# Performance work log

Measured on AMD Instinct MI355X. Metric: run time of the kernel, lower is better.

## Reference

```python
import jax, jax.numpy as jnp
import numpy as np


def _conv1x1(x_flat, W, b):
    # x_flat: [B, Cin, N], W: [Cout, Cin], b: [Cout]
    return jnp.einsum('oc,bcn->bon', W, x_flat) + b[None, :, None]


def setup_inputs() -> dict:
    key = jax.random.key(0)
    ks = jax.random.split(key, 7)
    B, C, H, W = 8, 64, 64, 64
    Ch = C // 2
    s_in = 1.0 / np.sqrt(C)
    x = jax.random.normal(ks[0], (B, C, H, W), dtype=jnp.float32)
    Wb = jax.random.uniform(ks[1], (Ch, C), jnp.float32, -s_in, s_in)
    bb = jax.random.uniform(ks[2], (Ch,), jnp.float32, -s_in, s_in)
    Wc = jax.random.uniform(ks[3], (Ch, C), jnp.float32, -s_in, s_in)
    bc = jax.random.uniform(ks[4], (Ch,), jnp.float32, -s_in, s_in)
    Wd = jax.random.uniform(ks[5], (C, C), jnp.float32, -s_in, s_in)
    bd = jax.random.uniform(ks[6], (C,), jnp.float32, -s_in, s_in)
    return {'x': x, 'Wb': Wb, 'bb': bb, 'Wc': Wc, 'bc': bc, 'Wd': Wd, 'bd': bd}


def reference(x, Wb, bb, Wc, bc, Wd, bd):
    B, C, H, Wd_ = x.shape
    N = H * Wd_
    x_flat = x.reshape(B, C, N)
    feat_b = _conv1x1(x_flat, Wb, bb)            # [B, C/2, N]
    feat_c = _conv1x1(x_flat, Wc, bc)            # [B, C/2, N]
    # scores[b,n,m] = sum_c feat_b[b,c,n] * feat_c[b,c,m]
    scores = jnp.einsum('bcn,bcm->bnm', feat_b, feat_c)
    attn = jax.nn.softmax(scores, axis=-1)       # [B, N, N]
    feat_d = _conv1x1(x_flat, Wd, bd)            # [B, C, N]
    # feat_e[b,c,m] = sum_n feat_d[b,c,n] * attn[b,m,n]  (bmm with attn^T)
    feat_e = jnp.einsum('bcn,bmn->bcm', feat_d, attn)
    return feat_e.reshape(B, C, H, Wd_) + x
```

## Files before the change

### kernel.cpp

```cpp
#include <hip/hip_runtime.h>

#define N_TOK 4096
#define L2E 1.44269504088896340736f

typedef short bf16x8 __attribute__((ext_vector_type(8)));
typedef float f32x4 __attribute__((ext_vector_type(4)));
typedef float f32x16 __attribute__((ext_vector_type(16)));
typedef unsigned int u32x4 __attribute__((ext_vector_type(4)));
typedef unsigned short u16x4 __attribute__((ext_vector_type(4)));

static __device__ __forceinline__ unsigned short f2bf(float f) {
    unsigned int u = __builtin_bit_cast(unsigned int, f);
    u += 0x7FFFu + ((u >> 16) & 1u);
    return (unsigned short)(u >> 16);
}
static __device__ __forceinline__ float bf2f(unsigned short v) {
    return __builtin_bit_cast(float, ((unsigned)v) << 16);
}

__global__ __launch_bounds__(256) void proj_kernel(
    const float* __restrict__ x,
    const float* __restrict__ Wb, const float* __restrict__ bb,
    const float* __restrict__ Wc, const float* __restrict__ bc,
    const float* __restrict__ Wd, const float* __restrict__ bd,
    unsigned short* __restrict__ Qg, unsigned short* __restrict__ Kg,
    unsigned short* __restrict__ VgT)
{
    const int b   = blockIdx.y;
    const int n0  = blockIdx.x * 64;
    const int tid = threadIdx.x;

    __shared__ unsigned short Wl[128 * 72];
    __shared__ unsigned short xT[64 * 72];
    __shared__ float bl[128];

    #pragma unroll
    for (int i = 0; i < 32; ++i) {
        int e = i * 256 + tid;
        int row = e >> 6, c = e & 63;
        float v;
        if (row < 32)      v = Wb[row * 64 + c];
        else if (row < 64) v = Wc[(row - 32) * 64 + c];
        else               v = Wd[(row - 64) * 64 + c];
        Wl[row * 72 + c] = f2bf(v);
    }
    if (tid < 128) {
        float v;
        if (tid < 32)      v = bb[tid];
        else if (tid < 64) v = bc[tid - 32];
        else               v = bd[tid - 64];
        bl[tid] = v;
    }
    #pragma unroll
    for (int i = 0; i < 16; ++i) {
        int e = i * 256 + tid;
        int c = e >> 6, nn = e & 63;
        xT[nn * 72 + c] = f2bf(x[((b * 64 + c) << 12) + n0 + nn]);
    }
    __syncthreads();

    const int w = tid >> 6, l = tid & 63;
    const int lrow = l & 15, lk = (l >> 4) * 8;

    const f32x4 vzero = {0.f, 0.f, 0.f, 0.f};
    f32x4 acc[2][4];
    #pragma unroll
    for (int rt = 0; rt < 2; ++rt)
        #pragma unroll
        for (int ct = 0; ct < 4; ++ct)
            acc[rt][ct] = vzero;

    #pragma unroll
    for (int kb = 0; kb < 2; ++kb) {
        bf16x8 af[2];
        #pragma unroll
        for (int rt = 0; rt < 2; ++rt)
            af[rt] = *(const bf16x8*)&Wl[(w * 32 + rt * 16 + lrow) * 72 + kb * 32 + lk];
        #pragma unroll
        for (int ct = 0; ct < 4; ++ct) {
            bf16x8 bfr = *(const bf16x8*)&xT[(ct * 16 + lrow) * 72 + kb * 32 + lk];
            #pragma unroll
            for (int rt = 0; rt < 2; ++rt)
                acc[rt][ct] = __builtin_amdgcn_mfma_f32_16x16x32_bf16(af[rt], bfr, acc[rt][ct], 0, 0, 0);
        }
    }

    #pragma unroll
    for (int rt = 0; rt < 2; ++rt) {
        const int row0 = w * 32 + rt * 16 + ((l >> 4) << 2);
        #pragma unroll
        for (int ct = 0; ct < 4; ++ct) {
            const int n = n0 + ct * 16 + lrow;
            if (row0 < 64) {
                u16x4 pk;
                #pragma unroll
                for (int r = 0; r < 4; ++r) {
                    float v = acc[rt][ct][r] + bl[row0 + r];
                    if (row0 < 32) v *= L2E;
                    pk[r] = f2bf(v);
                }
                unsigned short* dst = (row0 < 32)
                    ? Qg + (size_t)(b * N_TOK + n) * 32 + row0
                    : Kg + (size_t)(b * N_TOK + n) * 32 + (row0 - 32);
                *(u16x4*)dst = pk;
            } else {
                #pragma unroll
                for (int r = 0; r < 4; ++r)
                    VgT[((size_t)(b * 64 + row0 - 64 + r) << 12) + n] =
                        f2bf(acc[rt][ct][r] + bl[row0 + r]);
            }
        }
    }
}

template <int NHALF>
__global__ __launch_bounds__(256) void attn_kernel(
    const unsigned short* __restrict__ Qg,
    const unsigned short* __restrict__ Kg,
    const unsigned short* __restrict__ VgT,
    const float* __restrict__ x,
    float* __restrict__ outp,
    unsigned short* __restrict__ Opart,
    float* __restrict__ Ppart)
{
    const int nwg = 256 * NHALF;
    int i = blockIdx.x;
    int wg = (i & 7) * (nwg >> 3) + (i >> 3);
    const int b    = wg / (32 * NHALF);
    const int rem  = wg % (32 * NHALF);
    const int half = (NHALF >= 2) ? (rem >> 5) : 0;
    const int qblk = (NHALF >= 2) ? (rem & 31) : rem;
    const int q0   = qblk * 128;
    const int jbase = half * (N_TOK / NHALF);
    const int NT    = (N_TOK / NHALF) / 64;

    const int tid = threadIdx.x;
    const int w  = tid >> 6, l = tid & 63;
    const int lc = l & 31, hi = l >> 5;

    __shared__ __align__(16) unsigned short Kl[2][64 * 36];
    __shared__ __align__(16) unsigned short Vt[2][64 * 68];
    __shared__ float den[4][32];

    const unsigned short* qp = Qg + (size_t)(b * N_TOK + q0 + w * 32 + lc) * 32 + hi * 8;
    const bf16x8 qf0 = *(const bf16x8*)qp;
    const bf16x8 qf1 = *(const bf16x8*)(qp + 16);

    const int kj = tid >> 2, kseg = (tid & 3) * 8;
    const int vc = tid >> 2, vj   = (tid & 3) * 16;
    const size_t kbase = (size_t)(b * N_TOK + jbase + kj) * 32 + kseg;
    const size_t vbase = ((size_t)(b * 64 + vc) << 12) + jbase + vj;

    u32x4 kreg, vreg0, vreg1;

    kreg  = *(const u32x4*)&Kg[kbase];
    vreg0 = *(const u32x4*)&VgT[vbase];
    vreg1 = *(const u32x4*)&VgT[vbase + 8];
    *(u32x4*)&Kl[0][kj * 36 + kseg]   = kreg;
    *(u32x4*)&Vt[0][vc * 68 + vj]     = vreg0;
    *(u32x4*)&Vt[0][vc * 68 + vj + 8] = vreg1;
    if (NT > 1) {
        kreg  = *(const u32x4*)&Kg[kbase + 64 * 32];
        vreg0 = *(const u32x4*)&VgT[vbase + 64];
        vreg1 = *(const u32x4*)&VgT[vbase + 64 + 8];
    }
    __syncthreads();

    const f32x16 z16 = {0.f,0.f,0.f,0.f,0.f,0.f,0.f,0.f,0.f,0.f,0.f,0.f,0.f,0.f,0.f,0.f};
    f32x16 o0 = z16, o1 = z16;
    f32x16 s0, s1;
    float ps0 = 0.f, ps1 = 0.f;

    {
        __builtin_amdgcn_s_setprio(1);
        bf16x8 a00 = *(const bf16x8*)&Kl[0][(lc) * 36 + hi * 8];
        bf16x8 a01 = *(const bf16x8*)&Kl[0][(lc) * 36 + 16 + hi * 8];
        bf16x8 a10 = *(const bf16x8*)&Kl[0][(32 + lc) * 36 + hi * 8];
        bf16x8 a11 = *(const bf16x8*)&Kl[0][(32 + lc) * 36 + 16 + hi * 8];
        s0 = __builtin_amdgcn_mfma_f32_32x32x16_bf16(a00, qf0, z16, 0, 0, 0);
        s0 = __builtin_amdgcn_mfma_f32_32x32x16_bf16(a01, qf1, s0, 0, 0, 0);
        s1 = __builtin_amdgcn_mfma_f32_32x32x16_bf16(a10, qf0, z16, 0, 0, 0);
        s1 = __builtin_amdgcn_mfma_f32_32x32x16_bf16(a11, qf1, s1, 0, 0, 0);
        __builtin_amdgcn_s_setprio(0);
    }

    for (int t = 0; t < NT; ++t) {
        const int cur = t & 1;

        if (t + 1 < NT) {
            *(u32x4*)&Kl[cur ^ 1][kj * 36 + kseg]   = kreg;
            *(u32x4*)&Vt[cur ^ 1][vc * 68 + vj]     = vreg0;
            *(u32x4*)&Vt[cur ^ 1][vc * 68 + vj + 8] = vreg1;
        }
        if (t + 2 < NT) {
            const int j2 = (t + 2) * 64;
            kreg  = *(const u32x4*)&Kg[kbase + (size_t)j2 * 32];
            vreg0 = *(const u32x4*)&VgT[vbase + j2];
            vreg1 = *(const u32x4*)&VgT[vbase + j2 + 8];
        }

        #pragma unroll
        for (int kb = 0; kb < 4; ++kb) {
            const f32x16& sv = (kb >> 1) ? s1 : s0;
            const int e = (kb & 1) * 8;
            float p[8];
            #pragma unroll
            for (int r = 0; r < 8; ++r) {
                p[r] = __builtin_amdgcn_exp2f(sv[e + r]);
                if (r & 1) ps1 += p[r]; else ps0 += p[r];
            }
            unsigned A, B, C, D;
            asm("v_cvt_pk_bf16_f32 %0, %1, %2" : "=v"(A) : "v"(p[0]), "v"(p[1]));
            asm("v_cvt_pk_bf16_f32 %0, %1, %2" : "=v"(B) : "v"(p[2]), "v"(p[3]));
            asm("v_cvt_pk_bf16_f32 %0, %1, %2" : "=v"(C) : "v"(p[4]), "v"(p[5]));
            asm("v_cvt_pk_bf16_f32 %0, %1, %2" : "=v"(D) : "v"(p[6]), "v"(p[7]));
            asm("v_permlane32_swap_b32 %0, %1" : "+v"(A), "+v"(C));
            asm("v_permlane32_swap_b32 %0, %1" : "+v"(B), "+v"(D));
            u32x4 pw = {A, B, C, D};
            bf16x8 pf = __builtin_bit_cast(bf16x8, pw);
            bf16x8 vf0 = *(const bf16x8*)&Vt[cur][(lc) * 68 + kb * 16 + hi * 8];
            bf16x8 vf1 = *(const bf16x8*)&Vt[cur][(32 + lc) * 68 + kb * 16 + hi * 8];
            __builtin_amdgcn_s_setprio(1);
            o0 = __builtin_amdgcn_mfma_f32_32x32x16_bf16(pf, vf0, o0, 0, 0, 0);
            o1 = __builtin_amdgcn_mfma_f32_32x32x16_bf16(pf, vf1, o1, 0, 0, 0);
            __builtin_amdgcn_s_setprio(0);
        }

        __syncthreads();

        if (t + 1 < NT) {
            const int nxt = cur ^ 1;
            __builtin_amdgcn_s_setprio(1);
            bf16x8 a00 = *(const bf16x8*)&Kl[nxt][(lc) * 36 + hi * 8];
            bf16x8 a01 = *(const bf16x8*)&Kl[nxt][(lc) * 36 + 16 + hi * 8];
            bf16x8 a10 = *(const bf16x8*)&Kl[nxt][(32 + lc) * 36 + hi * 8];
            bf16x8 a11 = *(const bf16x8*)&Kl[nxt][(32 + lc) * 36 + 16 + hi * 8];
            s0 = __builtin_amdgcn_mfma_f32_32x32x16_bf16(a00, qf0, z16, 0, 0, 0);
            s0 = __builtin_amdgcn_mfma_f32_32x32x16_bf16(a01, qf1, s0, 0, 0, 0);
            s1 = __builtin_amdgcn_mfma_f32_32x32x16_bf16(a10, qf0, z16, 0, 0, 0);
            s1 = __builtin_amdgcn_mfma_f32_32x32x16_bf16(a11, qf1, s1, 0, 0, 0);
            __builtin_amdgcn_s_setprio(0);
        }
    }

    float ps = ps0 + ps1;
    float tot = ps + __shfl_xor(ps, 32, 64);

    if (NHALF == 1) {
        if (hi == 0) den[w][lc] = __builtin_amdgcn_rcpf(tot);
        __syncthreads();
        #pragma unroll
        for (int cb = 0; cb < 2; ++cb) {
            const f32x16& ov16 = cb ? o1 : o0;
            const int c = cb * 32 + lc;
            #pragma unroll
            for (int g2 = 0; g2 < 4; ++g2) {
                const int qb = q0 + w * 32 + g2 * 8 + hi * 4;
                f32x4 rinv = *(const f32x4*)&den[w][g2 * 8 + hi * 4];
                const size_t idx = (size_t)(b * 64 + c) * N_TOK + qb;
                f32x4 xv = *(const f32x4*)&x[idx];
                f32x4 ov;
                #pragma unroll
                for (int r = 0; r < 4; ++r)
                    ov[r] = ov16[g2 * 4 + r] * rinv[r] + xv[r];
                *(f32x4*)&outp[idx] = ov;
            }
        }
    } else {
        #pragma unroll
        for (int cb = 0; cb < 2; ++cb) {
            const f32x16& ov16 = cb ? o1 : o0;
            unsigned short* obase =
                Opart + ((size_t)((half * 8 + b) * 64 + cb * 32 + lc) << 12);
            #pragma unroll
            for (int g2 = 0; g2 < 4; ++g2) {
                const int qb = q0 + w * 32 + g2 * 8 + hi * 4;
                u16x4 pk;
                #pragma unroll
                for (int r = 0; r < 4; ++r) pk[r] = f2bf(ov16[g2 * 4 + r]);
                *(u16x4*)(obase + qb) = pk;
            }
        }
        if (hi == 0)
            Ppart[((size_t)(half * 8 + b) << 12) + q0 + w * 32 + lc] = tot;
    }
}

template <int NHALF>
__global__ __launch_bounds__(256) void combine_kernel(
    const unsigned short* __restrict__ Opart, const float* __restrict__ Ppart,
    const float* __restrict__ x, float* __restrict__ outp)
{
    const int i = blockIdx.x * 256 + threadIdx.x;
    const int q  = (i & 1023) << 2;
    const int bc = i >> 10;
    const int b  = bc >> 6;
    const size_t obase = ((size_t)bc << 12) + q;

    f32x4 osum = {0.f, 0.f, 0.f, 0.f};
    f32x4 psum = {0.f, 0.f, 0.f, 0.f};
    #pragma unroll
    for (int h = 0; h < NHALF; ++h) {
        u16x4 oh = *(const u16x4*)&Opart[(((size_t)(h * 512 + bc)) << 12) + q];
        f32x4 ph = *(const f32x4*)&Ppart[(((size_t)(h * 8 + b)) << 12) + q];
        #pragma unroll
        for (int r = 0; r < 4; ++r) { osum[r] += bf2f(oh[r]); psum[r] += ph[r]; }
    }
    f32x4 xv = *(const f32x4*)&x[obase];
    f32x4 ov;
    #pragma unroll
    for (int r = 0; r < 4; ++r)
        ov[r] = osum[r] * __builtin_amdgcn_rcpf(psum[r]) + xv[r];
    *(f32x4*)&outp[obase] = ov;
}

extern "C" void kernel_launch(void* const* d_in, const int* in_sizes, int n_in,
                              void* d_out, int out_size, void* d_ws, size_t ws_size,
                              hipStream_t stream) {
    const float* x  = (const float*)d_in[0];
    const float* Wb = (const float*)d_in[1];
    const float* bb = (const float*)d_in[2];
    const float* Wc = (const float*)d_in[3];
    const float* bc = (const float*)d_in[4];
    const float* Wd = (const float*)d_in[5];
    const float* bd = (const float*)d_in[6];
    float* out = (float*)d_out;

    unsigned short* Qg  = (unsigned short*)d_ws;
    unsigned short* Kg  = Qg + (size_t)8 * N_TOK * 32;
    unsigned short* VgT = Kg + (size_t)8 * N_TOK * 32;
    unsigned short* Opart = (unsigned short*)((char*)d_ws + (size_t)8 * 1024 * 1024);
    float* Ppart = (float*)((char*)d_ws + (size_t)24 * 1024 * 1024);

    proj_kernel<<<dim3(64, 8), 256, 0, stream>>>(x, Wb, bb, Wc, bc, Wd, bd, Qg, Kg, VgT);

    if (ws_size >= (size_t)25 * 1024 * 1024) {
        attn_kernel<2><<<512, 256, 0, stream>>>(Qg, Kg, VgT, x, out, Opart, Ppart);
        combine_kernel<2><<<2048, 256, 0, stream>>>(Opart, Ppart, x, out);
    } else {
        attn_kernel<1><<<256, 256, 0, stream>>>(Qg, Kg, VgT, x, out, nullptr, nullptr);
    }
}
```

Before: 57.55 us.

## Fuse split-KV combine into attention kernel via last-arriver atomic flag

Removes the separate combine kernel launch. Each of the two KV-half workgroups writes its partial output and denominator, then increments a per-(batch, query-block) counter. The second workgroup to arrive reads its partner's partial and produces the final normalized output plus residual. Flags are zeroed in the projection kernel. This saves a launch and one full read/write pass, at the cost of threadfence and atomic synchronization, and one half still writes partials it never needed to.

```diff
diff --git a/kernel.cpp b/kernel.cpp
--- a/kernel.cpp
+++ b/kernel.cpp
@@ -24,11 +24,14 @@
     const float* __restrict__ Wc, const float* __restrict__ bc,
     const float* __restrict__ Wd, const float* __restrict__ bd,
     unsigned short* __restrict__ Qg, unsigned short* __restrict__ Kg,
-    unsigned short* __restrict__ VgT)
+    unsigned short* __restrict__ VgT, int* __restrict__ flags)
 {
     const int b   = blockIdx.y;
     const int n0  = blockIdx.x * 64;
     const int tid = threadIdx.x;
+
+    if (flags && blockIdx.x == 0 && blockIdx.y == 0)
+        flags[tid] = 0;
 
     __shared__ unsigned short Wl[128 * 72];
     __shared__ unsigned short xT[64 * 72];
@@ -121,7 +124,8 @@
     const float* __restrict__ x,
     float* __restrict__ outp,
     unsigned short* __restrict__ Opart,
-    float* __restrict__ Ppart)
+    float* __restrict__ Ppart,
+    int* __restrict__ flags)
 {
     const int nwg = 256 * NHALF;
     int i = blockIdx.x;
@@ -141,6 +145,7 @@
     __shared__ __align__(16) unsigned short Kl[2][64 * 36];
     __shared__ __align__(16) unsigned short Vt[2][64 * 68];
     __shared__ float den[4][32];
+    __shared__ int soldv;
 
     const unsigned short* qp = Qg + (size_t)(b * N_TOK + q0 + w * 32 + lc) * 32 + hi * 8;
     const bf16x8 qf0 = *(const bf16x8*)qp;
@@ -283,35 +288,44 @@
         }
         if (hi == 0)
             Ppart[((size_t)(half * 8 + b) << 12) + q0 + w * 32 + lc] = tot;
-    }
-}
-
-template <int NHALF>
-__global__ __launch_bounds__(256) void combine_kernel(
-    const unsigned short* __restrict__ Opart, const float* __restrict__ Ppart,
-    const float* __restrict__ x, float* __restrict__ outp)
-{
-    const int i = blockIdx.x * 256 + threadIdx.x;
-    const int q  = (i & 1023) << 2;
-    const int bc = i >> 10;
-    const int b  = bc >> 6;
-    const size_t obase = ((size_t)bc << 12) + q;
-
-    f32x4 osum = {0.f, 0.f, 0.f, 0.f};
-    f32x4 psum = {0.f, 0.f, 0.f, 0.f};
-    #pragma unroll
-    for (int h = 0; h < NHALF; ++h) {
-        u16x4 oh = *(const u16x4*)&Opart[(((size_t)(h * 512 + bc)) << 12) + q];
-        f32x4 ph = *(const f32x4*)&Ppart[(((size_t)(h * 8 + b)) << 12) + q];
-        #pragma unroll
-        for (int r = 0; r < 4; ++r) { osum[r] += bf2f(oh[r]); psum[r] += ph[r]; }
-    }
-    f32x4 xv = *(const f32x4*)&x[obase];
-    f32x4 ov;
-    #pragma unroll
-    for (int r = 0; r < 4; ++r)
-        ov[r] = osum[r] * __builtin_amdgcn_rcpf(psum[r]) + xv[r];
-    *(f32x4*)&outp[obase] = ov;
+
+        __threadfence();
+        __syncthreads();
+        if (tid == 0) soldv = atomicAdd(&flags[b * 32 + qblk], 1);
+        __syncthreads();
+        if ((soldv & 1) == 0) return;
+        __threadfence();
+
+        const int oh = half ^ 1;
+        if (hi == 0) {
+            float totO = Ppart[((size_t)(oh * 8 + b) << 12) + q0 + w * 32 + lc];
+            den[w][lc] = __builtin_amdgcn_rcpf(tot + totO);
+        }
+        __syncthreads();
+
+        #pragma unroll
+        for (int cb = 0; cb < 2; ++cb) {
+            const f32x16& ov16 = cb ? o1 : o0;
+            const int c = cb * 32 + lc;
+            const unsigned short* obaseO =
+                Opart + ((size_t)((oh * 8 + b) * 64 + c) << 12);
+            #pragma unroll
+            for (int g2 = 0; g2 < 4; ++g2) {
+                const int qb = q0 + w * 32 + g2 * 8 + hi * 4;
+                u16x4 oth = *(const u16x4*)(obaseO + qb);
+                f32x4 rinv = *(const f32x4*)&den[w][g2 * 8 + hi * 4];
+                const size_t idx = (size_t)(b * 64 + c) * N_TOK + qb;
+                f32x4 xv = *(const f32x4*)&x[idx];
+                f32x4 ov;
+                #pragma unroll
+                for (int r = 0; r < 4; ++r) {
+                    float mine = bf2f(f2bf(ov16[g2 * 4 + r]));
+                    ov[r] = (mine + bf2f(oth[r])) * rinv[r] + xv[r];
+                }
+                *(f32x4*)&outp[idx] = ov;
+            }
+        }
+    }
 }
 
 extern "C" void kernel_launch(void* const* d_in, const int* in_sizes, int n_in,
@@ -331,13 +345,17 @@
     unsigned short* VgT = Kg + (size_t)8 * N_TOK * 32;
     unsigned short* Opart = (unsigned short*)((char*)d_ws + (size_t)8 * 1024 * 1024);
     float* Ppart = (float*)((char*)d_ws + (size_t)24 * 1024 * 1024);
-
-    proj_kernel<<<dim3(64, 8), 256, 0, stream>>>(x, Wb, bb, Wc, bc, Wd, bd, Qg, Kg, VgT);
-
-    if (ws_size >= (size_t)25 * 1024 * 1024) {
-        attn_kernel<2><<<512, 256, 0, stream>>>(Qg, Kg, VgT, x, out, Opart, Ppart);
-        combine_kernel<2><<<2048, 256, 0, stream>>>(Opart, Ppart, x, out);
+    int*   flags = (int*)((char*)d_ws + (size_t)24 * 1024 * 1024 + 512 * 1024);
+
+    const bool split = ws_size >= (size_t)25 * 1024 * 1024;
+
+    proj_kernel<<<dim3(64, 8), 256, 0, stream>>>(x, Wb, bb, Wc, bc, Wd, bd,
+                                                 Qg, Kg, VgT,
+                                                 split ? flags : nullptr);
+
+    if (split) {
+        attn_kernel<2><<<512, 256, 0, stream>>>(Qg, Kg, VgT, x, out, Opart, Ppart, flags);
     } else {
-        attn_kernel<1><<<256, 256, 0, stream>>>(Qg, Kg, VgT, x, out, nullptr, nullptr);
-    }
-}
+        attn_kernel<1><<<256, 256, 0, stream>>>(Qg, Kg, VgT, x, out, nullptr, nullptr, nullptr);
+    }
+}
```

After: 141.0 us. 145% more time.
